# Kernel tuning notes

Hardware: AMD Instinct MI355X
Metric: run time of the kernel (lower is better)

Reference implementation:

```python
import jax, jax.numpy as jnp
import numpy as np
from jax import lax

DIM = 1024
HEADS = 16
KERNEL = 7
STRIDE = 4
EPS = 1e-5


def setup_inputs() -> dict:
    key = jax.random.key(0)
    ks = jax.random.split(key, 4)
    B, N = 2, 4096
    w_scale = 0.02
    return {
        "x": jax.random.normal(ks[0], (B, N, DIM), dtype=jnp.float32),
        "ln_w": jnp.ones((DIM,), jnp.float32),
        "ln_b": jnp.zeros((DIM,), jnp.float32),
        "Wk": jax.random.normal(ks[1], (DIM, DIM, KERNEL), dtype=jnp.float32) * w_scale,
        "Wv": jax.random.normal(ks[2], (DIM, DIM, KERNEL), dtype=jnp.float32) * w_scale,
        "Wq": jax.random.normal(ks[3], (DIM, DIM, KERNEL), dtype=jnp.float32) * w_scale,
    }


def _conv1d(x_bnd, w):
    # x: (B, N, D) -> conv over sequence dim with 'same' padding; w: (out_ch, in_ch, K)
    x_cn = jnp.transpose(x_bnd, (0, 2, 1))  # (B, D, N)
    pad = KERNEL // 2
    y = lax.conv_general_dilated(
        x_cn, w, window_strides=(1,), padding=[(pad, pad)],
        dimension_numbers=("NCH", "OIH", "NCH"))
    return jnp.transpose(y, (0, 2, 1))  # (B, N, D)


def reference(x, ln_w, ln_b, Wk, Wv, Wq):
    B, N, D = x.shape
    hd = D // HEADS
    # LayerNorm (biased variance, as in torch)
    mu = jnp.mean(x, axis=-1, keepdims=True)
    var = jnp.mean(jnp.square(x - mu), axis=-1, keepdims=True)
    x_n = (x - mu) / jnp.sqrt(var + EPS) * ln_w + ln_b

    K = _conv1d(x_n, Wk)                 # (B, N, D)
    V = _conv1d(x_n, Wv)                 # (B, N, D)
    Q = _conv1d(x_n, Wq)[:, ::STRIDE]    # (B, M, D) windowed queries
    M = Q.shape[1]

    Qh = Q.reshape(B, M, HEADS, hd).transpose(0, 2, 1, 3)  # (B, H, M, hd)
    Kh = K.reshape(B, N, HEADS, hd).transpose(0, 2, 1, 3)  # (B, H, N, hd)
    Vh = V.reshape(B, N, HEADS, hd).transpose(0, 2, 1, 3)  # (B, H, N, hd)

    scale = jnp.sqrt(jnp.asarray(hd, x.dtype))
    scores = jnp.einsum("bhmd,bhnd->bhmn", Qh, Kh) / scale  # (B, H, M, N)
    attn = jax.nn.softmax(scores, axis=-1)
    out = jnp.einsum("bhmn,bhnd->bhmd", attn, Vh)           # (B, H, M, hd)
    out = out.transpose(0, 2, 1, 3).reshape(B, M, D)
    return out + Q
```

## Files before the change

kernel.cpp:

```cpp
#include <hip/hip_runtime.h>

typedef __attribute__((ext_vector_type(4))) float f32x4;
typedef __attribute__((ext_vector_type(8))) short short8;
typedef __attribute__((ext_vector_type(4))) unsigned short u16x4;

#define AS1 __attribute__((address_space(1)))
#define AS3 __attribute__((address_space(3)))

__device__ __forceinline__ unsigned short f2bf(float f) {
  unsigned u = __float_as_uint(f);
  return (unsigned short)((u + 0x7FFFu + ((u >> 16) & 1u)) >> 16);
}
__device__ __forceinline__ unsigned short f2bf_fast(float f) {
  return (unsigned short)((__float_as_uint(f) + 0x8000u) >> 16);
}

__global__ __launch_bounds__(256) void ln_kernel(
    const float* __restrict__ x, const float* __restrict__ lw,
    const float* __restrict__ lb, unsigned short* __restrict__ xpad) {
  __shared__ float red[8];
  int row = blockIdx.x;
  int b = row >> 12, n = row & 4095;
  const float* xr = x + (size_t)row * 1024;
  int c = threadIdx.x * 4;
  f32x4 v = *(const f32x4*)(xr + c);
  float s = v[0] + v[1] + v[2] + v[3];
  float sq = v[0]*v[0] + v[1]*v[1] + v[2]*v[2] + v[3]*v[3];
#pragma unroll
  for (int off = 32; off; off >>= 1) {
    s  += __shfl_xor(s, off, 64);
    sq += __shfl_xor(sq, off, 64);
  }
  int w = threadIdx.x >> 6;
  if ((threadIdx.x & 63) == 0) { red[w*2] = s; red[w*2+1] = sq; }
  __syncthreads();
  float S  = red[0]+red[2]+red[4]+red[6];
  float SQ = red[1]+red[3]+red[5]+red[7];
  float mean = S * (1.0f/1024.0f);
  float var  = SQ * (1.0f/1024.0f) - mean*mean;
  float rstd = rsqrtf(var + 1e-5f);
  f32x4 wv = *(const f32x4*)(lw + c);
  f32x4 bv = *(const f32x4*)(lb + c);
  u16x4 o;
#pragma unroll
  for (int r = 0; r < 4; ++r) o[r] = f2bf((v[r]-mean)*rstd*wv[r] + bv[r]);
  *(u16x4*)(xpad + (((size_t)(b*4102 + n + 3)) << 10) + c) = o;
}

__global__ __launch_bounds__(256) void repack_kernel(
    const float* __restrict__ Wk, const float* __restrict__ Wv,
    const float* __restrict__ Wq, unsigned short* __restrict__ Wt) {
  __shared__ unsigned short t[7168];
  const float* W = (blockIdx.y == 0) ? Wk : (blockIdx.y == 1) ? Wv : Wq;
  int o = blockIdx.x;
  const float* row = W + (size_t)o * 7168;
  unsigned short* orow = Wt + ((size_t)(blockIdx.y * 1024 + o)) * 7168;
#pragma unroll
  for (int p = 0; p < 7; ++p) {
    int idx = p*1024 + threadIdx.x*4;
    f32x4 v = *(const f32x4*)(row + idx);
#pragma unroll
    for (int e = 0; e < 4; ++e) {
      unsigned j = idx + e;
      unsigned i = (j * 149797u) >> 20;
      unsigned k = j - i*7;
      t[k*1024 + i] = f2bf(v[e]);
    }
  }
  __syncthreads();
#pragma unroll
  for (int p = 0; p < 7; ++p) {
    int idx = p*1024 + threadIdx.x*4;
    *(u16x4*)(orow + idx) = *(const u16x4*)(t + idx);
  }
}

__global__ __launch_bounds__(512, 2) void conv256(
    const unsigned short* __restrict__ Apad,
    const unsigned short* __restrict__ Wt,
    unsigned short* __restrict__ Ksg, unsigned short* __restrict__ Vsg,
    float* __restrict__ Qp) {
  __shared__ unsigned short As[2][2][8192];
  __shared__ unsigned short Bs[2][2][8192];

  const int tid = threadIdx.x;
  const int w = tid >> 6, l = tid & 63;
  const int wm = w >> 2, wn = w & 3;
  const int l15 = l & 15, lh4 = l >> 4, l7 = l & 7;
  const int chA = ((l7 & 4) | (lh4 ^ (l7 & 3))) << 3;
  const int wOff = w << 9;
  const int bid = blockIdx.x;
  const int ct = bid & 7, rt = bid >> 3;

  unsigned aOff[2][2], bOff[2][2];
#pragma unroll
  for (int i = 0; i < 2; ++i) {
    const int idx = i * 512 + tid;
    const int r = idx >> 3;
    const int clog8 = (((idx & 7) ^ (r & 7)) << 3);
#pragma unroll
    for (int hh = 0; hh < 2; ++hh) {
      const int rg = (rt << 8) + (hh << 7) + r;
      aOff[hh][i] = ((unsigned)((rg >> 12) * 4102 + (rg & 4095)) << 10) + clog8;
      const int cg = (ct << 8) + (hh << 7) + r;
      bOff[hh][i] = (unsigned)cg * 7168u + clog8;
    }
  }

  unsigned aRd[4], bRd[2];
#pragma unroll
  for (int fm = 0; fm < 4; ++fm)
    aRd[fm] = (unsigned)(((wm << 6) + (fm << 4) + l15) << 6) + chA;
#pragma unroll
  for (int fn = 0; fn < 2; ++fn)
    bRd[fn] = (unsigned)(((wn << 5) + (fn << 4) + l15) << 6) + chA;

  f32x4 acc[2][2][4][2] = {};
  short8 af[4][2], bfr[2][2];

#define STGA(BUF, HALF, T) do { \
    __builtin_amdgcn_global_load_lds((const AS1 void*)(Apad + aOff[HALF][0] + ((unsigned)(T) << 6)), (AS3 void*)&As[BUF][HALF][wOff], 16, 0, 0); \
    __builtin_amdgcn_global_load_lds((const AS1 void*)(Apad + aOff[HALF][1] + ((unsigned)(T) << 6)), (AS3 void*)&As[BUF][HALF][4096 + wOff], 16, 0, 0); \
  } while (0)
#define STGB(BUF, HALF, T) do { \
    __builtin_amdgcn_global_load_lds((const AS1 void*)(Wt + bOff[HALF][0] + ((unsigned)(T) << 6)), (AS3 void*)&Bs[BUF][HALF][wOff], 16, 0, 0); \
    __builtin_amdgcn_global_load_lds((const AS1 void*)(Wt + bOff[HALF][1] + ((unsigned)(T) << 6)), (AS3 void*)&Bs[BUF][HALF][4096 + wOff], 16, 0, 0); \
  } while (0)
#define LDA(BUF, MQ) do { \
    _Pragma("unroll") for (int fm = 0; fm < 4; ++fm) { \
      af[fm][0] = *(const short8*)&As[BUF][MQ][aRd[fm]]; \
      af[fm][1] = *(const short8*)&As[BUF][MQ][aRd[fm] ^ 32u]; } \
  } while (0)
#define LDB(BUF, NQ) do { \
    _Pragma("unroll") for (int fn = 0; fn < 2; ++fn) { \
      bfr[fn][0] = *(const short8*)&Bs[BUF][NQ][bRd[fn]]; \
      bfr[fn][1] = *(const short8*)&Bs[BUF][NQ][bRd[fn] ^ 32u]; } \
  } while (0)
#define MM(MQ, NQ) do { \
    _Pragma("unroll") for (int ks = 0; ks < 2; ++ks) \
    _Pragma("unroll") for (int fm = 0; fm < 4; ++fm) \
    _Pragma("unroll") for (int fn = 0; fn < 2; ++fn) \
      acc[MQ][NQ][fm][fn] = __builtin_amdgcn_mfma_f32_16x16x32_bf16(af[fm][ks], bfr[fn][ks], acc[MQ][NQ][fm][fn], 0, 0, 0); \
  } while (0)
#define BAR __builtin_amdgcn_s_barrier()
#define LGKM0 asm volatile("s_waitcnt lgkmcnt(0)" ::: "memory")
#define VM6 asm volatile("s_waitcnt vmcnt(6)" ::: "memory")
#define VM0 asm volatile("s_waitcnt vmcnt(0)" ::: "memory")
#define P1 __builtin_amdgcn_s_setprio(1)
#define P0 __builtin_amdgcn_s_setprio(0)

#define RUN_GEMM(NIT) do { \
    STGA(0, 0, 0); STGB(0, 0, 0); STGA(0, 1, 0); STGB(0, 1, 0); \
    STGA(1, 0, 1); STGB(1, 1, 1); STGA(1, 1, 1); \
    VM6; BAR; \
    for (int I = 0; I < (NIT) - 1; ++I) { \
      const int t0 = I * 2; \
      LDA(0, 0); LDB(0, 0); STGB(1, 0, t0 + 1); \
      BAR; LGKM0; P1; MM(0, 0); P0; BAR; \
      LDB(0, 1);            STGA(0, 0, t0 + 2); \
      BAR; LGKM0; P1; MM(0, 1); P0; BAR; \
      LDA(0, 1);            STGB(0, 1, t0 + 2); \
      BAR; LGKM0; P1; MM(1, 1); P0; BAR; \
      LDB(0, 0);            STGA(0, 1, t0 + 2); \
      BAR; LGKM0; P1; MM(1, 0); P0; VM6; BAR; \
      LDA(1, 0); LDB(1, 0); STGB(0, 0, t0 + 2); \
      BAR; LGKM0; P1; MM(0, 0); P0; BAR; \
      LDB(1, 1);            STGA(1, 0, t0 + 3); \
      BAR; LGKM0; P1; MM(0, 1); P0; BAR; \
      LDA(1, 1);            STGB(1, 1, t0 + 3); \
      BAR; LGKM0; P1; MM(1, 1); P0; BAR; \
      LDB(1, 0);            STGA(1, 1, t0 + 3); \
      BAR; LGKM0; P1; MM(1, 0); P0; VM6; BAR; \
    } \
    { \
      LDA(0, 0); LDB(0, 0); STGB(1, 0, ((NIT) - 1) * 2 + 1); \
      BAR; LGKM0; P1; MM(0, 0); P0; BAR; \
      LDB(0, 1); BAR; LGKM0; P1; MM(0, 1); P0; BAR; \
      LDA(0, 1); BAR; LGKM0; P1; MM(1, 1); P0; BAR; \
      LDB(0, 0); BAR; LGKM0; P1; MM(1, 0); P0; VM0; BAR; \
      LDA(1, 0); LDB(1, 0); BAR; LGKM0; P1; MM(0, 0); P0; BAR; \
      LDB(1, 1); BAR; LGKM0; P1; MM(0, 1); P0; BAR; \
      LDA(1, 1); BAR; LGKM0; P1; MM(1, 1); P0; BAR; \
      LDB(1, 0); BAR; LGKM0; P1; MM(1, 0); P0; BAR; \
    } \
  } while (0)

  RUN_GEMM(56);

  if (ct < 4) {
#pragma unroll
    for (int mq = 0; mq < 2; ++mq)
#pragma unroll
      for (int nq = 0; nq < 2; ++nq) {
        const int h = (ct << 2) + (nq << 1) + (wn >> 1);
        const int kd = wn & 1;
#pragma unroll
        for (int fm = 0; fm < 4; ++fm) {
          const int rbase = (rt << 8) + (mq << 7) + (wm << 6) + (fm << 4) + (lh4 << 2);
          const int b = rbase >> 12, n0 = rbase & 4095;
          const size_t base = ((((size_t)((b * 16 + h) * 2 + kd)) << 12) + n0) << 5;
#pragma unroll
          for (int fn = 0; fn < 2; ++fn) {
            const int d32 = (fn << 4) + l15;
#pragma unroll
            for (int rr = 0; rr < 4; ++rr)
              Ksg[base + ((size_t)rr << 5) + d32] = f2bf(acc[mq][nq][fm][fn][rr]);
          }
        }
      }
  } else {
#pragma unroll
    for (int mq = 0; mq < 2; ++mq)
#pragma unroll
      for (int nq = 0; nq < 2; ++nq) {
        const int h = ((ct - 4) << 2) + (nq << 1) + (wn >> 1);
        const int dhi = (wn & 1) << 5;
#pragma unroll
        for (int fm = 0; fm < 4; ++fm) {
          const int rbase = (rt << 8) + (mq << 7) + (wm << 6) + (fm << 4) + (lh4 << 2);
          const int b = rbase >> 12, n = rbase & 4095;
#pragma unroll
          for (int fn = 0; fn < 2; ++fn) {
            const int d = dhi + (fn << 4) + l15;
            const size_t rowbase =
                ((((((size_t)(b * 16 + h)) << 7) + (n >> 5)) << 6) + d) * 32 + (n & 31);
            u16x4 pv;
#pragma unroll
            for (int rr = 0; rr < 4; ++rr) pv[rr] = f2bf(acc[mq][nq][fm][fn][rr]);
            *(u16x4*)(Vsg + rowbase) = pv;
          }
        }
      }
  }

  const int qct = bid & 3, qrt = (bid >> 2) & 7, kc = bid >> 5;
  const unsigned kbase = (unsigned)kc * 896u;
#pragma unroll
  for (int i = 0; i < 2; ++i) {
    const int idx = i * 512 + tid;
    const int r = idx >> 3;
    const int clog8 = (((idx & 7) ^ (r & 7)) << 3);
#pragma unroll
    for (int hh = 0; hh < 2; ++hh) {
      const int rg = (qrt << 8) + (hh << 7) + r;
      aOff[hh][i] = ((unsigned)((rg >> 10) * 4102 + ((rg & 1023) << 2)) << 10) + clog8 + kbase;
      const int cg = 2048 + (qct << 8) + (hh << 7) + r;
      bOff[hh][i] = (unsigned)cg * 7168u + clog8 + kbase;
    }
  }
#pragma unroll
  for (int mq = 0; mq < 2; ++mq)
#pragma unroll
    for (int nq = 0; nq < 2; ++nq)
#pragma unroll
      for (int fm = 0; fm < 4; ++fm)
#pragma unroll
        for (int fn = 0; fn < 2; ++fn)
          acc[mq][nq][fm][fn] = (f32x4){0.f, 0.f, 0.f, 0.f};

  RUN_GEMM(7);

  float* Qc = Qp + ((size_t)kc << 21);
#pragma unroll
  for (int mq = 0; mq < 2; ++mq)
#pragma unroll
    for (int nq = 0; nq < 2; ++nq)
#pragma unroll
      for (int fm = 0; fm < 4; ++fm) {
        const int rq = (qrt << 8) + (mq << 7) + (wm << 6) + (fm << 4) + (lh4 << 2);
#pragma unroll
        for (int fn = 0; fn < 2; ++fn) {
          const int cq = (qct << 8) + (nq << 7) + (wn << 5) + (fn << 4) + l15;
#pragma unroll
          for (int rr = 0; rr < 4; ++rr)
            Qc[(((size_t)(rq + rr)) << 10) + cq] = acc[mq][nq][fm][fn][rr];
        }
      }
#undef STGA
#undef STGB
#undef LDA
#undef LDB
#undef MM
#undef BAR
#undef LGKM0
#undef VM6
#undef VM0
#undef P1
#undef P0
#undef RUN_GEMM
}

__global__ __launch_bounds__(256) void qfinal(
    const float* __restrict__ Qp, float* __restrict__ Qf,
    unsigned short* __restrict__ Qsg) {
  const int rq = blockIdx.x;
  const int b = rq >> 10, m = rq & 1023;
  const int c = threadIdx.x << 2;
  f32x4 v = {0.f, 0.f, 0.f, 0.f};
#pragma unroll
  for (int kc = 0; kc < 8; ++kc) {
    f32x4 p = *(const f32x4*)(Qp + ((size_t)kc << 21) + ((size_t)rq << 10) + c);
    v[0] += p[0]; v[1] += p[1]; v[2] += p[2]; v[3] += p[3];
  }
  *(f32x4*)(Qf + ((size_t)rq << 10) + c) = v;
  const int h = c >> 6, kd = (c >> 5) & 1, d32 = c & 31;
  u16x4 o;
#pragma unroll
  for (int e = 0; e < 4; ++e) o[e] = f2bf(v[e]);
  *(u16x4*)(Qsg + ((((size_t)((b * 16 + h) * 2 + kd)) << 10) + m) * 32 + d32) = o;
}

__global__ __launch_bounds__(256) void attn_kernel(
    const unsigned short* __restrict__ Ksg, const unsigned short* __restrict__ Vsg,
    const unsigned short* __restrict__ Qsg, const float* __restrict__ Qf,
    float* __restrict__ out) {
  __shared__ unsigned short Ks[8192];
  __shared__ unsigned short Vs[8192];
  __shared__ unsigned short Qs[4096];
  __shared__ unsigned short Ps[8704];
  const int tid = threadIdx.x, w = tid >> 6, l = tid & 63;
  const int g = blockIdx.x;
  const int bh = (g & 7) + (((g >> 3) & 3) << 3);
  const int qt = g >> 5;
  const int b = bh >> 4, h = bh & 15;
  const int m0 = qt << 6;
  const int quad = l >> 4, lc = l & 15, l3 = l & 3;
  const float C = 0.18033688011112042f;
  const int lsw = (l & 60) | ((l ^ (l >> 2)) & 3);

  const unsigned short* KgT = Ksg + ((size_t)bh << 18);
  const unsigned short* VgT = Vsg + ((size_t)bh << 18);
  const unsigned short* QgT = Qsg + ((size_t)bh << 16);

#pragma unroll
  for (int p = 0; p < 2; ++p) {
    int t = w*2 + p;
    int kd = t >> 2, ml = (t & 3) << 4;
    __builtin_amdgcn_global_load_lds(
        (const AS1 void*)(QgT + ((size_t)((kd << 10) + m0 + ml) << 5) + lsw*8),
        (AS3 void*)(Qs + (t << 9)), 16, 0, 0);
  }

  float l_run = 0.f;
  f32x4 oacc[4] = {};
  unsigned short* Pw = Ps + w*2176;

  for (int it = 0; it < 32; ++it) {
    int n0 = it << 7;
    __syncthreads();
#pragma unroll
    for (int p = 0; p < 4; ++p) {
      int t = (w << 2) + p;
      __builtin_amdgcn_global_load_lds(
          (const AS1 void*)(KgT + ((size_t)(((t >> 3) << 12) + n0 + ((t & 7) << 4)) << 5) + lsw*8),
          (AS3 void*)(Ks + (t << 9)), 16, 0, 0);
      __builtin_amdgcn_global_load_lds(
          (const AS1 void*)(VgT + ((size_t)((((n0 >> 5) + (t >> 2)) << 6) + ((t & 3) << 4)) << 5) + lsw*8),
          (AS3 void*)(Vs + (t << 9)), 16, 0, 0);
    }
    __syncthreads();

    const int ch = (quad ^ l3) << 3;
    short8 ak[8][2];
#pragma unroll
    for (int k = 0; k < 2; ++k)
#pragma unroll
      for (int ni = 0; ni < 8; ++ni)
        ak[ni][k] = *(const short8*)(Ks + (k << 12) + ((ni<<4) + lc)*32 + ch);

    f32x4 sv[8] = {};
#pragma unroll
    for (int k = 0; k < 2; ++k) {
      short8 bq = *(const short8*)(Qs + (k << 11) + ((w<<4) + lc)*32 + ch);
#pragma unroll
      for (int ni = 0; ni < 8; ++ni)
        sv[ni] = __builtin_amdgcn_mfma_f32_16x16x32_bf16(ak[ni][k], bq, sv[ni], 0, 0, 0);
    }

    float su = 0.f;
#pragma unroll
    for (int ni = 0; ni < 8; ++ni) {
      u16x4 pv;
#pragma unroll
      for (int rr = 0; rr < 4; ++rr) {
        float pp = __builtin_amdgcn_exp2f(sv[ni][rr] * C);
        su += pp;
        pv[rr] = f2bf_fast(pp);
      }
      *(u16x4*)(Pw + lc*136 + (ni<<4) + (quad<<2)) = pv;
    }
    su += __shfl_xor(su, 16, 64);
    su += __shfl_xor(su, 32, 64);
    l_run += su;

#pragma unroll
    for (int kn = 0; kn < 4; ++kn) {
      short8 bp = *(const short8*)(Pw + lc*136 + (kn<<5) + (quad<<3));
#pragma unroll
      for (int dt = 0; dt < 4; ++dt) {
        short8 av = *(const short8*)(Vs + (kn << 11) + ((dt<<4) + lc)*32 + ch);
        oacc[dt] = __builtin_amdgcn_mfma_f32_16x16x32_bf16(av, bp, oacc[dt], 0, 0, 0);
      }
    }
  }

  float invl = 1.0f / l_run;
  int m = m0 + (w<<4) + lc;
#pragma unroll
  for (int dt = 0; dt < 4; ++dt) {
    int d = (dt<<4) + (quad<<2);
    size_t off = (((size_t)(b << 10) + m) << 10) + (h << 6) + d;
    f32x4 qv = *(const f32x4*)(Qf + off);
    f32x4 ov;
#pragma unroll
    for (int rr = 0; rr < 4; ++rr) ov[rr] = oacc[dt][rr]*invl + qv[rr];
    *(f32x4*)(out + off) = ov;
  }
}

extern "C" void kernel_launch(void* const* d_in, const int* in_sizes, int n_in,
                              void* d_out, int out_size, void* d_ws, size_t ws_size,
                              hipStream_t stream) {
  const float* x  = (const float*)d_in[0];
  const float* lw = (const float*)d_in[1];
  const float* lb = (const float*)d_in[2];
  const float* Wk = (const float*)d_in[3];
  const float* Wv = (const float*)d_in[4];
  const float* Wq = (const float*)d_in[5];
  float* out = (float*)d_out;

  char* ws = (char*)d_ws;
  size_t off = 0;
  unsigned short* xpad = (unsigned short*)(ws + off); off += (size_t)2*4102*1024*2;
  unsigned short* Wt   = (unsigned short*)(ws + off); off += (size_t)3072*7168*2;
  unsigned short* Ksg  = (unsigned short*)(ws + off); off += (size_t)32*2*4096*32*2;
  unsigned short* Vsg  = (unsigned short*)(ws + off); off += (size_t)32*128*64*32*2;
  unsigned short* Qsg  = (unsigned short*)(ws + off); off += (size_t)32*2*1024*32*2;
  float*          Qf   = (float*)(ws + off);          off += (size_t)2048*1024*4;
  float*          Qp   = (float*)(ws + off);          off += (size_t)8*2048*1024*4;

  for (int b = 0; b < 2; ++b) {
    hipMemsetAsync(xpad + (size_t)b*4102*1024, 0, 3*1024*2, stream);
    hipMemsetAsync(xpad + ((size_t)b*4102 + 4099)*1024, 0, 3*1024*2, stream);
  }
  ln_kernel<<<dim3(8192), dim3(256), 0, stream>>>(x, lw, lb, xpad);
  repack_kernel<<<dim3(1024, 3), dim3(256), 0, stream>>>(Wk, Wv, Wq, Wt);
  conv256<<<dim3(256), dim3(512), 0, stream>>>(xpad, Wt, Ksg, Vsg, Qp);
  qfinal<<<dim3(2048), dim3(256), 0, stream>>>(Qp, Qf, Qsg);
  attn_kernel<<<dim3(512), dim3(256), 0, stream>>>(Ksg, Vsg, Qsg, Qf, out);
}
```

Baseline: 507.1 us.

## Double-buffer K/V in attention with larger query tiles; remap conv blocks per XCD

The attention kernel now runs 512 threads per block over 128 queries instead of 64, which halves the grid. K/V tiles are double-buffered in LDS, so the next tile's global-to-LDS loads are issued before computing on the current one. This replaces the two full barriers per iteration with one waitcnt-plus-barrier at the end of each iteration. The conv kernel's block index is remapped so blocks on the same XCD share row tiles and Q-split chunks, aiming for better L2 locality. The costs are much higher LDS use per block and fewer, larger blocks, which could lower occupancy or leave some CUs underused.

```diff
diff --git a/kernel.cpp b/kernel.cpp
--- a/kernel.cpp
+++ b/kernel.cpp
@@ -90,7 +90,8 @@
   const int chA = ((l7 & 4) | (lh4 ^ (l7 & 3))) << 3;
   const int wOff = w << 9;
   const int bid = blockIdx.x;
-  const int ct = bid & 7, rt = bid >> 3;
+  const int xcd = bid & 7, j = bid >> 3;
+  const int ct = j & 7, rt = (xcd << 2) | (j >> 3);
 
   unsigned aOff[2][2], bOff[2][2];
 #pragma unroll
@@ -233,7 +234,7 @@
       }
   }
 
-  const int qct = bid & 3, qrt = (bid >> 2) & 7, kc = bid >> 5;
+  const int qct = j & 3, qrt = j >> 2, kc = xcd;
   const unsigned kbase = (unsigned)kc * 896u;
 #pragma unroll
   for (int i = 0; i < 2; ++i) {
@@ -310,20 +311,20 @@
   *(u16x4*)(Qsg + ((((size_t)((b * 16 + h) * 2 + kd)) << 10) + m) * 32 + d32) = o;
 }
 
-__global__ __launch_bounds__(256) void attn_kernel(
+__global__ __launch_bounds__(512) void attn_kernel(
     const unsigned short* __restrict__ Ksg, const unsigned short* __restrict__ Vsg,
     const unsigned short* __restrict__ Qsg, const float* __restrict__ Qf,
     float* __restrict__ out) {
-  __shared__ unsigned short Ks[8192];
-  __shared__ unsigned short Vs[8192];
-  __shared__ unsigned short Qs[4096];
-  __shared__ unsigned short Ps[8704];
+  __shared__ unsigned short Ks[2][8192];
+  __shared__ unsigned short Vs[2][8192];
+  __shared__ unsigned short Qs[8192];
+  __shared__ unsigned short Ps[17408];
   const int tid = threadIdx.x, w = tid >> 6, l = tid & 63;
   const int g = blockIdx.x;
   const int bh = (g & 7) + (((g >> 3) & 3) << 3);
   const int qt = g >> 5;
   const int b = bh >> 4, h = bh & 15;
-  const int m0 = qt << 6;
+  const int m0 = qt << 7;
   const int quad = l >> 4, lc = l & 15, l3 = l & 3;
   const float C = 0.18033688011112042f;
   const int lsw = (l & 60) | ((l ^ (l >> 2)) & 3);
@@ -334,31 +335,38 @@
 
 #pragma unroll
   for (int p = 0; p < 2; ++p) {
-    int t = w*2 + p;
-    int kd = t >> 2, ml = (t & 3) << 4;
+    int t = (w << 1) + p;
+    int kd = t >> 3, ml = (t & 7) << 4;
     __builtin_amdgcn_global_load_lds(
         (const AS1 void*)(QgT + ((size_t)((kd << 10) + m0 + ml) << 5) + lsw*8),
         (AS3 void*)(Qs + (t << 9)), 16, 0, 0);
   }
 
+#define STAGE_KV(BUF, N0) do { \
+    _Pragma("unroll") for (int p = 0; p < 2; ++p) { \
+      int t = (w << 1) + p; \
+      __builtin_amdgcn_global_load_lds( \
+          (const AS1 void*)(KgT + ((size_t)(((t >> 3) << 12) + (N0) + ((t & 7) << 4)) << 5) + lsw*8), \
+          (AS3 void*)(Ks[BUF] + (t << 9)), 16, 0, 0); \
+      __builtin_amdgcn_global_load_lds( \
+          (const AS1 void*)(VgT + ((size_t)(((((N0) >> 5) + (t >> 2)) << 6) + ((t & 3) << 4)) << 5) + lsw*8), \
+          (AS3 void*)(Vs[BUF] + (t << 9)), 16, 0, 0); \
+    } \
+  } while (0)
+
   float l_run = 0.f;
   f32x4 oacc[4] = {};
   unsigned short* Pw = Ps + w*2176;
 
+  STAGE_KV(0, 0);
+  asm volatile("s_waitcnt vmcnt(0)" ::: "memory");
+  __builtin_amdgcn_s_barrier();
+
   for (int it = 0; it < 32; ++it) {
-    int n0 = it << 7;
-    __syncthreads();
-#pragma unroll
-    for (int p = 0; p < 4; ++p) {
-      int t = (w << 2) + p;
-      __builtin_amdgcn_global_load_lds(
-          (const AS1 void*)(KgT + ((size_t)(((t >> 3) << 12) + n0 + ((t & 7) << 4)) << 5) + lsw*8),
-          (AS3 void*)(Ks + (t << 9)), 16, 0, 0);
-      __builtin_amdgcn_global_load_lds(
-          (const AS1 void*)(VgT + ((size_t)((((n0 >> 5) + (t >> 2)) << 6) + ((t & 3) << 4)) << 5) + lsw*8),
-          (AS3 void*)(Vs + (t << 9)), 16, 0, 0);
-    }
-    __syncthreads();
+    const int cur = it & 1;
+    if (it < 31) STAGE_KV(cur ^ 1, (it + 1) << 7);
+    const unsigned short* Kc = Ks[cur];
+    const unsigned short* Vc = Vs[cur];
 
     const int ch = (quad ^ l3) << 3;
     short8 ak[8][2];
@@ -366,12 +374,12 @@
     for (int k = 0; k < 2; ++k)
 #pragma unroll
       for (int ni = 0; ni < 8; ++ni)
-        ak[ni][k] = *(const short8*)(Ks + (k << 12) + ((ni<<4) + lc)*32 + ch);
+        ak[ni][k] = *(const short8*)(Kc + (k << 12) + ((ni<<4) + lc)*32 + ch);
 
     f32x4 sv[8] = {};
 #pragma unroll
     for (int k = 0; k < 2; ++k) {
-      short8 bq = *(const short8*)(Qs + (k << 11) + ((w<<4) + lc)*32 + ch);
+      short8 bq = *(const short8*)(Qs + (k << 12) + ((w<<4) + lc)*32 + ch);
 #pragma unroll
       for (int ni = 0; ni < 8; ++ni)
         sv[ni] = __builtin_amdgcn_mfma_f32_16x16x32_bf16(ak[ni][k], bq, sv[ni], 0, 0, 0);
@@ -398,11 +406,15 @@
       short8 bp = *(const short8*)(Pw + lc*136 + (kn<<5) + (quad<<3));
 #pragma unroll
       for (int dt = 0; dt < 4; ++dt) {
-        short8 av = *(const short8*)(Vs + (kn << 11) + ((dt<<4) + lc)*32 + ch);
+        short8 av = *(const short8*)(Vc + (kn << 11) + ((dt<<4) + lc)*32 + ch);
         oacc[dt] = __builtin_amdgcn_mfma_f32_16x16x32_bf16(av, bp, oacc[dt], 0, 0, 0);
       }
     }
-  }
+
+    asm volatile("s_waitcnt vmcnt(0)" ::: "memory");
+    __builtin_amdgcn_s_barrier();
+  }
+#undef STAGE_KV
 
   float invl = 1.0f / l_run;
   int m = m0 + (w<<4) + lc;
@@ -447,5 +459,5 @@
   repack_kernel<<<dim3(1024, 3), dim3(256), 0, stream>>>(Wk, Wv, Wq, Wt);
   conv256<<<dim3(256), dim3(512), 0, stream>>>(xpad, Wt, Ksg, Vsg, Qp);
   qfinal<<<dim3(2048), dim3(256), 0, stream>>>(Qp, Qf, Qsg);
-  attn_kernel<<<dim3(512), dim3(256), 0, stream>>>(Ksg, Vsg, Qsg, Qf, out);
-}
+  attn_kernel<<<dim3(256), dim3(512), 0, stream>>>(Ksg, Vsg, Qsg, Qf, out);
+}
```

After: 479.8 us. -5.4%, faster.
